# Kernel tuning notes

Measured on AMD Instinct MI355X. Metric: run time of the kernel, lower is better.

The kernel has to match this reference:

```python
import jax, jax.numpy as jnp
import numpy as np

B, C, H, W = 8, 64, 64, 64
T, G, HID = 8, 8, 64


def setup_inputs() -> dict:
    key = jax.random.key(0)
    ks = jax.random.split(key, 8)
    s = 0.05
    return {
        "h": jax.random.normal(ks[0], (B, C, H, W), jnp.float32),
        "w_in": jax.random.normal(ks[1], (G * T, C), jnp.float32) * s,
        "b_in": jnp.zeros((G * T,), jnp.float32),
        "w_ih": jax.random.normal(ks[2], (4 * HID, 1), jnp.float32) * s,
        "w_hh": jax.random.normal(ks[3], (4 * HID, HID), jnp.float32) * s,
        "b_ih": jnp.zeros((4 * HID,), jnp.float32),
        "b_hh": jnp.zeros((4 * HID,), jnp.float32),
        "w_s": jax.random.normal(ks[4], (1, HID), jnp.float32) * s,
        "b_s": jnp.zeros((1,), jnp.float32),
        "w_out": jax.random.normal(ks[5], (C, G * T), jnp.float32) * s,
        "b_out": jnp.zeros((C,), jnp.float32),
    }


def reference(h, w_in, b_in, w_ih, w_hh, b_ih, b_hh, w_s, b_s, w_out, b_out):
    Bb, Cc, Hh, Ww = h.shape
    # 1x1 conv in-projection: (B,C,H,W) -> (B,G*T,H,W)
    y = jnp.einsum('bchw,oc->bohw', h, w_in) + b_in[None, :, None, None]
    y = y.reshape(Bb, G, T, Hh, Ww)
    # (B,G,H,W,T) -> (N,T) scalar sequences
    seq = jnp.transpose(y, (0, 1, 3, 4, 2)).reshape(-1, T)
    N = seq.shape[0]
    xs = seq.T  # (T, N) time-major for scan
    bias = b_ih + b_hh  # (4H,)
    w_x = w_ih[:, 0]    # (4H,) scalar-input weights

    def step(carry, x_t):
        hprev, cprev = carry
        # gates: i, f, g, o in torch LSTM ordering
        gates = x_t[:, None] * w_x[None, :] + hprev @ w_hh.T + bias  # (N,4H)
        i, f, g, o = jnp.split(gates, 4, axis=1)
        i = jax.nn.sigmoid(i)
        f = jax.nn.sigmoid(f)
        o = jax.nn.sigmoid(o)
        g = jnp.tanh(g)
        c = f * cprev + i * g
        hn = o * jnp.tanh(c)
        s_t = hn @ w_s[0] + b_s[0]  # fused to_scalar: (N,)
        return (hn, c), s_t

    init = (jnp.zeros((N, HID), h.dtype), jnp.zeros((N, HID), h.dtype))
    _, s = jax.lax.scan(step, init, xs)  # s: (T, N)

    out = s.T.reshape(Bb, G, Hh, Ww, T)
    out = jnp.transpose(out, (0, 1, 4, 2, 3)).reshape(Bb, G * T, Hh, Ww)
    # 1x1 conv out-projection back to C channels
    out = jnp.einsum('bchw,oc->bohw', out, w_out) + b_out[None, :, None, None]
    return out
```

## Files before the change

kernel.cpp:

```cpp
#include <hip/hip_runtime.h>
#include <hip/hip_bf16.h>

#define HW    4096
#define BB    8
#define TT    8

constexpr int OFF_WFRAG = 0;
constexpr int OFF_WXB   = 12800;

constexpr float SI = -1.44269504088896340736f;
constexpr float SG =  2.88539008177792681472f;

typedef _Float16 halfx8 __attribute__((ext_vector_type(8)));
typedef _Float16 halfx4 __attribute__((ext_vector_type(4)));
typedef float    floatx4 __attribute__((ext_vector_type(4)));
typedef float    floatx2 __attribute__((ext_vector_type(2)));

__device__ inline float fast_exp2(float x) {
#if __has_builtin(__builtin_amdgcn_exp2f)
    return __builtin_amdgcn_exp2f(x);
#else
    return __builtin_exp2f(x);
#endif
}
__device__ inline float fast_rcp(float x) {
#if __has_builtin(__builtin_amdgcn_rcpf)
    return __builtin_amdgcn_rcpf(x);
#else
    return 1.0f / x;
#endif
}
__device__ inline floatx2 exp2x2(floatx2 x) {
    floatx2 r; r.x = fast_exp2(x.x); r.y = fast_exp2(x.y); return r;
}
__device__ inline floatx2 rcpx2(floatx2 x) {
    float R = fast_rcp(x.x * x.y);
    floatx2 r; r.x = R * x.y; r.y = R * x.x; return r;
}

union pack8 { _Float16 h[8]; uint4 u; };

__global__ __launch_bounds__(256) void prep_kernel(
    const float* __restrict__ w_ih,  const float* __restrict__ w_hh,
    const float* __restrict__ b_ih,  const float* __restrict__ b_hh,
    const float* __restrict__ w_s,   const float* __restrict__ w_out,
    float* __restrict__ ws_f) {
    int tid = threadIdx.x;
    int bid = blockIdx.x;
    if (bid < 9) {
        int e = bid * 256 + tid;
        uint4* wf = (uint4*)(ws_f + OFF_WFRAG);
        if (e < 2048) {
            int l  = e & 63;
            int fi = e >> 6;
            int nb = fi >> 1, kc = fi & 1;
            int hb = nb & 3, gi = nb >> 2;
            int gate = gi * 64 + 4 * (l & 15) + hb;
            int hid  = kc * 32 + (l >> 4) * 8;
            float sc = (gi == 2) ? SG : SI;
            const float* src = w_hh + gate * 64 + hid;
            pack8 p;
            #pragma unroll
            for (int j = 0; j < 8; ++j) p.h[j] = (_Float16)(src[j] * sc);
            wf[e] = p.u;
        } else if (e < 2176) {
            int t2 = e - 2048;
            int l = t2 & 63, kc = t2 >> 6;
            pack8 p;
            #pragma unroll
            for (int j = 0; j < 8; ++j) p.h[j] = (_Float16)0.0f;
            if ((l & 15) == 0) {
                #pragma unroll
                for (int j = 0; j < 8; ++j)
                    p.h[j] = (_Float16)w_s[kc * 32 + (l >> 4) * 8 + j];
            }
            wf[e] = p.u;
        }
    } else {
        int s_ = tid & 15, hb = (tid >> 4) & 3, gi = tid >> 6;
        int gate = gi * 64 + 4 * s_ + hb;
        float sc = (gi == 2) ? SG : SI;
        floatx2 v; v.x = w_ih[gate] * sc; v.y = (b_ih[gate] + b_hh[gate]) * sc;
        ((floatx2*)(ws_f + OFF_WXB))[tid] = v;
    }
}

__global__ __launch_bounds__(1024) void lstm_kernel(
    const float* __restrict__ hin,
    const float* __restrict__ ws_f,
    float* __restrict__ out,
    const float* __restrict__ w_in,
    const float* __restrict__ b_in,
    const float* __restrict__ b_s_p,
    const float* __restrict__ b_out,
    const float* __restrict__ w_out) {
    __shared__ uint4 wfrag_lds[2176];
    __shared__ floatx2 wxb_lds[256];
    __shared__ __align__(16) float xs_buf[2048];
    __shared__ __align__(16) _Float16 h_lds[16384];

    int tid = threadIdx.x;
    int lane = tid & 63;
    int wv   = tid >> 6;
    int tl   = wv >> 3;
    int g    = wv & 7;
    int s    = lane & 15;
    int q    = lane >> 4;

    int gt = blockIdx.x * 2 + tl;
    int b  = gt >> 8;
    int p0 = (gt & 255) * 16;

    const uint4* wfg = (const uint4*)(ws_f + OFF_WFRAG);
    #pragma unroll
    for (int i = 0; i < 3; ++i) {
        int e = tid + 1024 * i;
        if (e < 2176) wfrag_lds[e] = wfg[e];
    }
    if (tid < 256) wxb_lds[tid] = ((const floatx2*)(ws_f + OFF_WXB))[tid];
    if (tid < 512) {
        int tls = tid >> 8, cc = (tid >> 2) & 63, f4 = tid & 3;
        int gts = blockIdx.x * 2 + tls;
        int bs_ = gts >> 8, p0s = (gts & 255) * 16;
        ((floatx4*)h_lds)[tid] =
            *(const floatx4*)&hin[(bs_ * 64 + cc) * HW + p0s + f4 * 4];
    }
    __syncthreads();

    float* xs = xs_buf + tl * 1024 + g * 128;
    {
        const float* hin_st = (const float*)h_lds + tl * 1024;
        const float* wrow0 = w_in + (g * 8 + q) * 64;
        const float* wrow1 = w_in + (g * 8 + q + 4) * 64;
        floatx2 xacc; xacc.x = b_in[g * 8 + q]; xacc.y = b_in[g * 8 + q + 4];
        #pragma unroll 8
        for (int cc = 0; cc < 64; ++cc) {
            float hv = hin_st[cc * 16 + s];
            xacc.x += wrow0[cc] * hv;
            xacc.y += wrow1[cc] * hv;
        }
        xs[q * 16 + s]       = xacc.x;
        xs[(q + 4) * 16 + s] = xacc.y;
    }
    __syncthreads();
    #pragma unroll
    for (int i = 0; i < 8; ++i)
        ((unsigned*)h_lds)[tid + 1024 * i] = 0u;
    __syncthreads();

    _Float16* hrow = h_lds + wv * 1024;
    float bs = b_s_p[0];
    int sh8 = (s >> 1);
    int so4 = 4 * (s & 1);

    float c_st[4][4];
    #pragma unroll
    for (int hb = 0; hb < 4; ++hb)
        #pragma unroll
        for (int r = 0; r < 4; ++r) c_st[hb][r] = 0.0f;

    for (int t = 0; t < TT; ++t) {
        asm volatile("" ::: "memory");

        halfx8 a0 = *(const halfx8*)(hrow + s * 64 + 8 * (q ^ (s & 7)));
        halfx8 a1 = *(const halfx8*)(hrow + s * 64 + 8 * ((q + 4) ^ (s & 7)));

        if (t > 0) {
            halfx8 sb0 = *(const halfx8*)&wfrag_lds[32 * 64 + lane];
            halfx8 sb1 = *(const halfx8*)&wfrag_lds[33 * 64 + lane];
            floatx4 sa = {0.f, 0.f, 0.f, 0.f};
            sa = __builtin_amdgcn_mfma_f32_16x16x32_f16(a0, sb0, sa, 0, 0, 0);
            sa = __builtin_amdgcn_mfma_f32_16x16x32_f16(a1, sb1, sa, 0, 0, 0);
            if (s == 0) {
                floatx4 o4 = {sa[0] + bs, sa[1] + bs, sa[2] + bs, sa[3] + bs};
                *(floatx4*)&xs[(t - 1) * 16 + q * 4] = o4;
            }
        }

        floatx4 xv = *(const floatx4*)&xs[t * 16 + q * 4];
        floatx2 xlo; xlo.x = xv[0]; xlo.y = xv[1];
        floatx2 xhi; xhi.x = xv[2]; xhi.y = xv[3];

        halfx4 hpack[4];

        #pragma unroll
        for (int hb = 0; hb < 4; ++hb) {
            floatx4 acc[4];
            #pragma unroll
            for (int gi = 0; gi < 4; ++gi) {
                int nb = hb + 4 * gi;
                floatx2 wb = wxb_lds[s + 16 * nb];
                floatx2 lo = xlo * wb.x + wb.y;
                floatx2 hi = xhi * wb.x + wb.y;
                floatx4 a = {lo.x, lo.y, hi.x, hi.y};
                halfx8 b0 = *(const halfx8*)&wfrag_lds[(nb * 2 + 0) * 64 + lane];
                halfx8 b1 = *(const halfx8*)&wfrag_lds[(nb * 2 + 1) * 64 + lane];
                a = __builtin_amdgcn_mfma_f32_16x16x32_f16(a0, b0, a, 0, 0, 0);
                a = __builtin_amdgcn_mfma_f32_16x16x32_f16(a1, b1, a, 0, 0, 0);
                acc[gi] = a;
            }
            #pragma unroll
            for (int p = 0; p < 2; ++p) {
                int r0 = 2 * p;
                floatx2 Ei; Ei.x = fast_exp2(acc[0][r0]); Ei.y = fast_exp2(acc[0][r0 + 1]);
                floatx2 Ef; Ef.x = fast_exp2(acc[1][r0]); Ef.y = fast_exp2(acc[1][r0 + 1]);
                floatx2 Eg; Eg.x = fast_exp2(acc[2][r0]); Eg.y = fast_exp2(acc[2][r0 + 1]);
                floatx2 Eo; Eo.x = fast_exp2(acc[3][r0]); Eo.y = fast_exp2(acc[3][r0 + 1]);
                floatx2 Bf  = Ef + 1.0f;
                floatx2 Pig = (Ei + 1.0f) * (Eg + 1.0f);
                floatx2 cp; cp.x = c_st[hb][r0]; cp.y = c_st[hb][r0 + 1];
                floatx2 num = cp * Pig + (Eg * SG - SG) * Bf;
                floatx2 cs  = num * rcpx2(Bf * Pig);
                c_st[hb][r0] = cs.x; c_st[hb][r0 + 1] = cs.y;
                floatx2 Ec  = exp2x2(cs);
                floatx2 hn  = (Ec - 1.0f) * rcpx2((Eo + 1.0f) * (Ec + 1.0f));
                hpack[r0 + 0][hb] = (_Float16)hn.x;
                hpack[r0 + 1][hb] = (_Float16)hn.y;
            }
        }
        {
            int rowb = q * 4;
            #pragma unroll
            for (int r = 0; r < 4; ++r) {
                int row = rowb + r;
                *(halfx4*)(hrow + row * 64 + 8 * (sh8 ^ (row & 7)) + so4) = hpack[r];
            }
        }
    }
    {
        asm volatile("" ::: "memory");
        halfx8 a0 = *(const halfx8*)(hrow + s * 64 + 8 * (q ^ (s & 7)));
        halfx8 a1 = *(const halfx8*)(hrow + s * 64 + 8 * ((q + 4) ^ (s & 7)));
        halfx8 sb0 = *(const halfx8*)&wfrag_lds[32 * 64 + lane];
        halfx8 sb1 = *(const halfx8*)&wfrag_lds[33 * 64 + lane];
        floatx4 sa = {0.f, 0.f, 0.f, 0.f};
        sa = __builtin_amdgcn_mfma_f32_16x16x32_f16(a0, sb0, sa, 0, 0, 0);
        sa = __builtin_amdgcn_mfma_f32_16x16x32_f16(a1, sb1, sa, 0, 0, 0);
        if (s == 0) {
            floatx4 o4 = {sa[0] + bs, sa[1] + bs, sa[2] + bs, sa[3] + bs};
            *(floatx4*)&xs[7 * 16 + q * 4] = o4;
        }
    }
    __syncthreads();

    {
        int tle = tid >> 9;
        int px  = tid & 15;
        int oo  = (tid >> 4) & 31;
        int gte = blockIdx.x * 2 + tle;
        int be  = gte >> 8, p0e = (gte & 255) * 16;
        const float* st = xs_buf + tle * 1024;
        floatx2 acc; acc.x = b_out[oo]; acc.y = b_out[oo + 32];
        #pragma unroll
        for (int c4 = 0; c4 < 16; ++c4) {
            floatx4 w0 = *(const floatx4*)&w_out[oo * 64 + c4 * 4];
            floatx4 w1 = *(const floatx4*)&w_out[(oo + 32) * 64 + c4 * 4];
            #pragma unroll
            for (int j = 0; j < 4; ++j) {
                float sv = st[(c4 * 4 + j) * 16 + px];
                acc.x += w0[j] * sv;
                acc.y += w1[j] * sv;
            }
        }
        out[(be * 64 + oo) * HW + p0e + px]      = acc.x;
        out[(be * 64 + oo + 32) * HW + p0e + px] = acc.y;
    }
}

extern "C" void kernel_launch(void* const* d_in, const int* in_sizes, int n_in,
                              void* d_out, int out_size, void* d_ws, size_t ws_size,
                              hipStream_t stream) {
    const float* h     = (const float*)d_in[0];
    const float* w_in  = (const float*)d_in[1];
    const float* b_in  = (const float*)d_in[2];
    const float* w_ih  = (const float*)d_in[3];
    const float* w_hh  = (const float*)d_in[4];
    const float* b_ih  = (const float*)d_in[5];
    const float* b_hh  = (const float*)d_in[6];
    const float* w_s   = (const float*)d_in[7];
    const float* b_s   = (const float*)d_in[8];
    const float* w_out = (const float*)d_in[9];
    const float* b_out = (const float*)d_in[10];
    float* out = (float*)d_out;
    float* ws  = (float*)d_ws;

    prep_kernel<<<10, 256, 0, stream>>>(w_ih, w_hh, b_ih, b_hh, w_s, w_out, ws);
    lstm_kernel<<<1024, 1024, 0, stream>>>(h, ws, out, w_in, b_in, b_s, b_out, w_out);
}
```

Baseline: 246.5 us.

## Halve LSTM block size, keep to_scalar weights in registers, pack gate input weights as fp16

Each block now processes one 16-pixel tile with 512 threads instead of two tiles with 1024 threads. The grid doubles to 2048 blocks and LDS per block drops by roughly half, which should improve occupancy and scheduling granularity. The w_s fragments are built directly in registers rather than read from LDS every timestep. The input-weight/bias pairs are stored as packed fp16, and the w_in loads are vectorized. The risks are extra register pressure from the held fragments, repeated weight staging per block, and precision loss in the fp16 input weights and bias.

```diff
diff --git a/kernel.cpp b/kernel.cpp
--- a/kernel.cpp
+++ b/kernel.cpp
@@ -6,7 +6,7 @@
 #define TT    8
 
 constexpr int OFF_WFRAG = 0;
-constexpr int OFF_WXB   = 12800;
+constexpr int OFF_WXB   = 8192;
 
 constexpr float SI = -1.44269504088896340736f;
 constexpr float SG =  2.88539008177792681472f;
@@ -39,105 +39,109 @@
 }
 
 union pack8 { _Float16 h[8]; uint4 u; };
+union uh2   { unsigned u; _Float16 h[2]; };
 
 __global__ __launch_bounds__(256) void prep_kernel(
     const float* __restrict__ w_ih,  const float* __restrict__ w_hh,
     const float* __restrict__ b_ih,  const float* __restrict__ b_hh,
-    const float* __restrict__ w_s,   const float* __restrict__ w_out,
     float* __restrict__ ws_f) {
     int tid = threadIdx.x;
     int bid = blockIdx.x;
-    if (bid < 9) {
+    if (bid < 8) {
         int e = bid * 256 + tid;
         uint4* wf = (uint4*)(ws_f + OFF_WFRAG);
-        if (e < 2048) {
-            int l  = e & 63;
-            int fi = e >> 6;
-            int nb = fi >> 1, kc = fi & 1;
-            int hb = nb & 3, gi = nb >> 2;
-            int gate = gi * 64 + 4 * (l & 15) + hb;
-            int hid  = kc * 32 + (l >> 4) * 8;
-            float sc = (gi == 2) ? SG : SI;
-            const float* src = w_hh + gate * 64 + hid;
-            pack8 p;
-            #pragma unroll
-            for (int j = 0; j < 8; ++j) p.h[j] = (_Float16)(src[j] * sc);
-            wf[e] = p.u;
-        } else if (e < 2176) {
-            int t2 = e - 2048;
-            int l = t2 & 63, kc = t2 >> 6;
-            pack8 p;
-            #pragma unroll
-            for (int j = 0; j < 8; ++j) p.h[j] = (_Float16)0.0f;
-            if ((l & 15) == 0) {
-                #pragma unroll
-                for (int j = 0; j < 8; ++j)
-                    p.h[j] = (_Float16)w_s[kc * 32 + (l >> 4) * 8 + j];
-            }
-            wf[e] = p.u;
-        }
+        int l  = e & 63;
+        int fi = e >> 6;
+        int nb = fi >> 1, kc = fi & 1;
+        int hb = nb & 3, gi = nb >> 2;
+        int gate = gi * 64 + 4 * (l & 15) + hb;
+        int hid  = kc * 32 + (l >> 4) * 8;
+        float sc = (gi == 2) ? SG : SI;
+        const float* src = w_hh + gate * 64 + hid;
+        pack8 p;
+        #pragma unroll
+        for (int j = 0; j < 8; ++j) p.h[j] = (_Float16)(src[j] * sc);
+        wf[e] = p.u;
     } else {
         int s_ = tid & 15, hb = (tid >> 4) & 3, gi = tid >> 6;
         int gate = gi * 64 + 4 * s_ + hb;
         float sc = (gi == 2) ? SG : SI;
-        floatx2 v; v.x = w_ih[gate] * sc; v.y = (b_ih[gate] + b_hh[gate]) * sc;
-        ((floatx2*)(ws_f + OFF_WXB))[tid] = v;
-    }
-}
-
-__global__ __launch_bounds__(1024) void lstm_kernel(
+        uh2 v;
+        v.h[0] = (_Float16)(w_ih[gate] * sc);
+        v.h[1] = (_Float16)((b_ih[gate] + b_hh[gate]) * sc);
+        ((unsigned*)(ws_f + OFF_WXB))[tid] = v.u;
+    }
+}
+
+__global__ __launch_bounds__(512) void lstm_kernel(
     const float* __restrict__ hin,
     const float* __restrict__ ws_f,
     float* __restrict__ out,
     const float* __restrict__ w_in,
     const float* __restrict__ b_in,
+    const float* __restrict__ w_s,
     const float* __restrict__ b_s_p,
     const float* __restrict__ b_out,
     const float* __restrict__ w_out) {
-    __shared__ uint4 wfrag_lds[2176];
-    __shared__ floatx2 wxb_lds[256];
-    __shared__ __align__(16) float xs_buf[2048];
-    __shared__ __align__(16) _Float16 h_lds[16384];
+    __shared__ uint4 wfrag_lds[2048];
+    __shared__ unsigned wxb_lds[256];
+    __shared__ __align__(16) float xs_buf[1024];
+    __shared__ __align__(16) _Float16 h_lds[8192];
 
     int tid = threadIdx.x;
+    int ptile = blockIdx.x & 255;
+    int b     = blockIdx.x >> 8;
+    int p0 = ptile * 16;
+
     int lane = tid & 63;
     int wv   = tid >> 6;
-    int tl   = wv >> 3;
-    int g    = wv & 7;
+    int g    = wv;
     int s    = lane & 15;
     int q    = lane >> 4;
 
-    int gt = blockIdx.x * 2 + tl;
-    int b  = gt >> 8;
-    int p0 = (gt & 255) * 16;
-
     const uint4* wfg = (const uint4*)(ws_f + OFF_WFRAG);
     #pragma unroll
-    for (int i = 0; i < 3; ++i) {
-        int e = tid + 1024 * i;
-        if (e < 2176) wfrag_lds[e] = wfg[e];
-    }
-    if (tid < 256) wxb_lds[tid] = ((const floatx2*)(ws_f + OFF_WXB))[tid];
-    if (tid < 512) {
-        int tls = tid >> 8, cc = (tid >> 2) & 63, f4 = tid & 3;
-        int gts = blockIdx.x * 2 + tls;
-        int bs_ = gts >> 8, p0s = (gts & 255) * 16;
-        ((floatx4*)h_lds)[tid] =
-            *(const floatx4*)&hin[(bs_ * 64 + cc) * HW + p0s + f4 * 4];
-    }
-    __syncthreads();
-
-    float* xs = xs_buf + tl * 1024 + g * 128;
+    for (int i = 0; i < 4; ++i)
+        wfrag_lds[tid + 512 * i] = wfg[tid + 512 * i];
+    if (tid < 256) wxb_lds[tid] = ((const unsigned*)(ws_f + OFF_WXB))[tid];
+    if (tid < 256) {
+        int cc = tid >> 2, f4 = tid & 3;
+        ((floatx4*)h_lds)[tid] = *(const floatx4*)&hin[(b * 64 + cc) * HW + p0 + f4 * 4];
+    }
+    halfx8 sb0, sb1;
+    #pragma unroll
+    for (int j = 0; j < 8; ++j) { sb0[j] = (_Float16)0.0f; sb1[j] = (_Float16)0.0f; }
+    if (s == 0) {
+        floatx4 v0 = *(const floatx4*)&w_s[q * 8];
+        floatx4 v1 = *(const floatx4*)&w_s[q * 8 + 4];
+        floatx4 v2 = *(const floatx4*)&w_s[32 + q * 8];
+        floatx4 v3 = *(const floatx4*)&w_s[32 + q * 8 + 4];
+        #pragma unroll
+        for (int j = 0; j < 4; ++j) {
+            sb0[j]     = (_Float16)v0[j];
+            sb0[4 + j] = (_Float16)v1[j];
+            sb1[j]     = (_Float16)v2[j];
+            sb1[4 + j] = (_Float16)v3[j];
+        }
+    }
+    __syncthreads();
+
+    float* xs = xs_buf + g * 128;
     {
-        const float* hin_st = (const float*)h_lds + tl * 1024;
-        const float* wrow0 = w_in + (g * 8 + q) * 64;
-        const float* wrow1 = w_in + (g * 8 + q + 4) * 64;
+        const float* hin_st = (const float*)h_lds;
+        const floatx4* w0p = (const floatx4*)(w_in + (g * 8 + q) * 64);
+        const floatx4* w1p = (const floatx4*)(w_in + (g * 8 + q + 4) * 64);
         floatx2 xacc; xacc.x = b_in[g * 8 + q]; xacc.y = b_in[g * 8 + q + 4];
-        #pragma unroll 8
-        for (int cc = 0; cc < 64; ++cc) {
-            float hv = hin_st[cc * 16 + s];
-            xacc.x += wrow0[cc] * hv;
-            xacc.y += wrow1[cc] * hv;
+        #pragma unroll 4
+        for (int c4 = 0; c4 < 16; ++c4) {
+            floatx4 wv0 = w0p[c4];
+            floatx4 wv1 = w1p[c4];
+            #pragma unroll
+            for (int j = 0; j < 4; ++j) {
+                float hv = hin_st[(c4 * 4 + j) * 16 + s];
+                xacc.x += wv0[j] * hv;
+                xacc.y += wv1[j] * hv;
+            }
         }
         xs[q * 16 + s]       = xacc.x;
         xs[(q + 4) * 16 + s] = xacc.y;
@@ -145,7 +149,7 @@
     __syncthreads();
     #pragma unroll
     for (int i = 0; i < 8; ++i)
-        ((unsigned*)h_lds)[tid + 1024 * i] = 0u;
+        ((unsigned*)h_lds)[tid + 512 * i] = 0u;
     __syncthreads();
 
     _Float16* hrow = h_lds + wv * 1024;
@@ -166,8 +170,6 @@
         halfx8 a1 = *(const halfx8*)(hrow + s * 64 + 8 * ((q + 4) ^ (s & 7)));
 
         if (t > 0) {
-            halfx8 sb0 = *(const halfx8*)&wfrag_lds[32 * 64 + lane];
-            halfx8 sb1 = *(const halfx8*)&wfrag_lds[33 * 64 + lane];
             floatx4 sa = {0.f, 0.f, 0.f, 0.f};
             sa = __builtin_amdgcn_mfma_f32_16x16x32_f16(a0, sb0, sa, 0, 0, 0);
             sa = __builtin_amdgcn_mfma_f32_16x16x32_f16(a1, sb1, sa, 0, 0, 0);
@@ -189,9 +191,11 @@
             #pragma unroll
             for (int gi = 0; gi < 4; ++gi) {
                 int nb = hb + 4 * gi;
-                floatx2 wb = wxb_lds[s + 16 * nb];
-                floatx2 lo = xlo * wb.x + wb.y;
-                floatx2 hi = xhi * wb.x + wb.y;
+                uh2 wb; wb.u = wxb_lds[s + 16 * nb];
+                float wx = (float)wb.h[0];
+                float bi = (float)wb.h[1];
+                floatx2 lo = xlo * wx + bi;
+                floatx2 hi = xhi * wx + bi;
                 floatx4 a = {lo.x, lo.y, hi.x, hi.y};
                 halfx8 b0 = *(const halfx8*)&wfrag_lds[(nb * 2 + 0) * 64 + lane];
                 halfx8 b1 = *(const halfx8*)&wfrag_lds[(nb * 2 + 1) * 64 + lane];
@@ -231,8 +235,6 @@
         asm volatile("" ::: "memory");
         halfx8 a0 = *(const halfx8*)(hrow + s * 64 + 8 * (q ^ (s & 7)));
         halfx8 a1 = *(const halfx8*)(hrow + s * 64 + 8 * ((q + 4) ^ (s & 7)));
-        halfx8 sb0 = *(const halfx8*)&wfrag_lds[32 * 64 + lane];
-        halfx8 sb1 = *(const halfx8*)&wfrag_lds[33 * 64 + lane];
         floatx4 sa = {0.f, 0.f, 0.f, 0.f};
         sa = __builtin_amdgcn_mfma_f32_16x16x32_f16(a0, sb0, sa, 0, 0, 0);
         sa = __builtin_amdgcn_mfma_f32_16x16x32_f16(a1, sb1, sa, 0, 0, 0);
@@ -244,12 +246,8 @@
     __syncthreads();
 
     {
-        int tle = tid >> 9;
-        int px  = tid & 15;
-        int oo  = (tid >> 4) & 31;
-        int gte = blockIdx.x * 2 + tle;
-        int be  = gte >> 8, p0e = (gte & 255) * 16;
-        const float* st = xs_buf + tle * 1024;
+        int px = tid & 15;
+        int oo = tid >> 4;
         floatx2 acc; acc.x = b_out[oo]; acc.y = b_out[oo + 32];
         #pragma unroll
         for (int c4 = 0; c4 < 16; ++c4) {
@@ -257,13 +255,13 @@
             floatx4 w1 = *(const floatx4*)&w_out[(oo + 32) * 64 + c4 * 4];
             #pragma unroll
             for (int j = 0; j < 4; ++j) {
-                float sv = st[(c4 * 4 + j) * 16 + px];
+                float sv = xs_buf[(c4 * 4 + j) * 16 + px];
                 acc.x += w0[j] * sv;
                 acc.y += w1[j] * sv;
             }
         }
-        out[(be * 64 + oo) * HW + p0e + px]      = acc.x;
-        out[(be * 64 + oo + 32) * HW + p0e + px] = acc.y;
+        out[(b * 64 + oo) * HW + p0 + px]      = acc.x;
+        out[(b * 64 + oo + 32) * HW + p0 + px] = acc.y;
     }
 }
 
@@ -284,6 +282,7 @@
     float* out = (float*)d_out;
     float* ws  = (float*)d_ws;
 
-    prep_kernel<<<10, 256, 0, stream>>>(w_ih, w_hh, b_ih, b_hh, w_s, w_out, ws);
-    lstm_kernel<<<1024, 1024, 0, stream>>>(h, ws, out, w_in, b_in, b_s, b_out, w_out);
-}
+    prep_kernel<<<9, 256, 0, stream>>>(w_ih, w_hh, b_ih, b_hh, ws);
+    lstm_kernel<<<2048, 512, 0, stream>>>(h, ws, out, w_in, b_in, w_s, b_s,
+                                          b_out, w_out);
+}
```

Result: faster. 232.1 us (-5.8%).
